# Kernel optimization log

Measured on AMD Instinct MI355X. Metric: run time of the kernel, lower is better.

## Reference

```python
import jax, jax.numpy as jnp
import numpy as np


def setup_inputs() -> dict:
    key = jax.random.key(0)
    kq, kk, kv = jax.random.split(key, 3)
    B, S, D = 16, 2048, 128
    q = jax.random.normal(kq, (B, S, D), dtype=jnp.float32)
    k = jax.random.normal(kk, (B, S, D), dtype=jnp.float32)
    v = jax.random.normal(kv, (B, S, D), dtype=jnp.float32)
    return {"q": q, "k": k, "v": v}


def reference(q, k, v):
    # q: (B, Sq, Dk), k: (B, Skv, Dk), v: (B, Skv, Dv)
    d_k = k.shape[-1]
    scale = 1.0 / jnp.sqrt(jnp.asarray(d_k, dtype=q.dtype))
    scores = jnp.einsum("bqd,bkd->bqk", q, k) * scale  # (B, Sq, Skv)
    # causal mask: strictly-upper-triangular positions set to -inf (mask=True in init)
    Sq = q.shape[-2]
    causal = jnp.triu(jnp.ones((Sq, Sq), dtype=bool), k=1)
    scores = jnp.where(causal, -jnp.inf, scores)
    attn = jax.nn.softmax(scores, axis=-1)
    return jnp.einsum("bqk,bkd->bqd", attn, v)
```

## Files before the change

kernel.cpp:

```cpp
#include <hip/hip_runtime.h>
#include <hip/hip_bf16.h>

typedef __bf16 bf16;
typedef bf16 bf16x8 __attribute__((ext_vector_type(8)));
typedef bf16 bf16x4 __attribute__((ext_vector_type(4)));
typedef float f32x4 __attribute__((ext_vector_type(4)));

#define DHEAD 128
#define SCL2 0.1275500811965365f
#define NINF (-__builtin_inff())

__device__ __forceinline__ unsigned pk2(float a, float b) {
  bf16 x = (bf16)a, y = (bf16)b;
  unsigned short ux = __builtin_bit_cast(unsigned short, x);
  unsigned short uy = __builtin_bit_cast(unsigned short, y);
  return ((unsigned)uy << 16) | (unsigned)ux;
}

__global__ __launch_bounds__(256) void fa_fwd(
    const float* __restrict__ Q, const float* __restrict__ K,
    const float* __restrict__ V, float* __restrict__ O, int S)
{
  const int bid = blockIdx.x;
  const int prb = bid & 255;
  const int hb  = bid >> 8;
  const int b   = prb & 15;
  const int jj  = prb >> 4;
  const int qt  = hb ? jj : (31 - jj);

  const int tid  = threadIdx.x;
  const int wave = tid >> 6;
  const int lane = tid & 63;
  const int lr   = lane & 15;
  const int lg   = lane >> 4;

  __shared__ bf16 Ks[2][32][136];
  __shared__ bf16 Vt[2][DHEAD][40];
  __shared__ bf16 Ps[4][16][40];

  const size_t bo = (size_t)b * S * DHEAD;
  const float* Qb = Q + bo + (size_t)qt * 64 * DHEAD;
  const float* Kb = K + bo;
  const float* Vb = V + bo;
  const int wrow0 = qt * 64 + wave * 16;

  const int j   = tid & 31;
  const int prw = tid >> 5;
  const int d4  = j << 2;
  const int Gw  = (j >> 1) & 3;

  bf16x8 qf[4];
  {
    const float* qr = Qb + (size_t)(wave * 16 + lr) * DHEAD;
    #pragma unroll
    for (int c = 0; c < 4; ++c) {
      const float4 u0 = *reinterpret_cast<const float4*>(qr + c * 32 + lg * 8);
      const float4 u1 = *reinterpret_cast<const float4*>(qr + c * 32 + lg * 8 + 4);
      bf16x8 f;
      f[0] = (bf16)u0.x; f[1] = (bf16)u0.y; f[2] = (bf16)u0.z; f[3] = (bf16)u0.w;
      f[4] = (bf16)u1.x; f[5] = (bf16)u1.y; f[6] = (bf16)u1.z; f[7] = (bf16)u1.w;
      qf[c] = f;
    }
  }

  f32x4 oacc[8];
  #pragma unroll
  for (int i = 0; i < 8; ++i) oacc[i] = (f32x4){0.f, 0.f, 0.f, 0.f};
  float m = NINF, l = 0.f;

  const int nt = 2 * (qt + 1);
  float4 kA[2], kB[2], vA[2], vB[2];

  auto load_tile = [&](int kc) {
    #pragma unroll
    for (int ps = 0; ps < 2; ++ps) {
      const int kv = kc + 2 * (prw + 8 * ps);
      const float* kp = Kb + (size_t)kv * DHEAD + d4;
      const float* vp = Vb + (size_t)kv * DHEAD + d4;
      kA[ps] = *reinterpret_cast<const float4*>(kp);
      kB[ps] = *reinterpret_cast<const float4*>(kp + DHEAD);
      vA[ps] = *reinterpret_cast<const float4*>(vp);
      vB[ps] = *reinterpret_cast<const float4*>(vp + DHEAD);
    }
  };
  auto write_tile = [&](int buf) {
    #pragma unroll
    for (int ps = 0; ps < 2; ++ps) {
      const int kvp = prw + 8 * ps;
      bf16x4 ka, kb;
      ka[0] = (bf16)kA[ps].x; ka[1] = (bf16)kA[ps].y;
      ka[2] = (bf16)kA[ps].z; ka[3] = (bf16)kA[ps].w;
      kb[0] = (bf16)kB[ps].x; kb[1] = (bf16)kB[ps].y;
      kb[2] = (bf16)kB[ps].z; kb[3] = (bf16)kB[ps].w;
      *reinterpret_cast<bf16x4*>(&Ks[buf][2 * kvp][d4])     = ka;
      *reinterpret_cast<bf16x4*>(&Ks[buf][2 * kvp + 1][d4]) = kb;
      const int pS = kvp ^ (Gw << 2);
      const float* fa = &vA[ps].x;
      const float* fb = &vB[ps].x;
      #pragma unroll
      for (int c = 0; c < 4; ++c) {
        *reinterpret_cast<unsigned*>(&Vt[buf][d4 + c][2 * pS]) = pk2(fa[c], fb[c]);
      }
    }
  };

  load_tile(0);
  write_tile(0);
  if (nt > 1) load_tile(32);

  int cur = 0;
  for (int t = 0; t < nt; ++t) {
    __syncthreads();
    if (t + 1 < nt) write_tile(cur ^ 1);
    if (t + 2 < nt) load_tile((t + 2) * 32);

    const int kc = t * 32;
    if (kc <= wrow0 + 15) {
      f32x4 s0 = {0.f, 0.f, 0.f, 0.f}, s1 = {0.f, 0.f, 0.f, 0.f};
      __builtin_amdgcn_s_setprio(1);
      #pragma unroll
      for (int c = 0; c < 4; ++c) {
        const bf16x8 kf0 = *reinterpret_cast<const bf16x8*>(&Ks[cur][lr][c * 32 + lg * 8]);
        const bf16x8 kf1 = *reinterpret_cast<const bf16x8*>(&Ks[cur][16 + lr][c * 32 + lg * 8]);
        s0 = __builtin_amdgcn_mfma_f32_16x16x32_bf16(kf0, qf[c], s0, 0, 0, 0);
        s1 = __builtin_amdgcn_mfma_f32_16x16x32_bf16(kf1, qf[c], s1, 0, 0, 0);
      }
      __builtin_amdgcn_s_setprio(0);

      const int qg = wrow0 + lr;
      float x0[4], x1[4];
      if (kc + 31 > wrow0) {
        #pragma unroll
        for (int r = 0; r < 4; ++r) {
          x0[r] = (kc + 4 * lg + r      > qg) ? NINF : s0[r] * SCL2;
          x1[r] = (kc + 16 + 4 * lg + r > qg) ? NINF : s1[r] * SCL2;
        }
      } else {
        #pragma unroll
        for (int r = 0; r < 4; ++r) { x0[r] = s0[r] * SCL2; x1[r] = s1[r] * SCL2; }
      }
      float tm = NINF;
      #pragma unroll
      for (int r = 0; r < 4; ++r) tm = fmaxf(tm, fmaxf(x0[r], x1[r]));
      tm = fmaxf(tm, __shfl_xor(tm, 16));
      tm = fmaxf(tm, __shfl_xor(tm, 32));

      if (!__all(tm <= m + 8.0f)) {
        const float mn = fmaxf(m, tm);
        const float al = __builtin_exp2f(m - mn);
        m = mn; l *= al;
        #pragma unroll
        for (int r = 0; r < 4; ++r) {
          const float ar = __shfl(al, 4 * lg + r);
          #pragma unroll
          for (int ds = 0; ds < 8; ++ds) oacc[ds][r] *= ar;
        }
      }

      float p0[4], p1[4];
      float ts = 0.f;
      #pragma unroll
      for (int r = 0; r < 4; ++r) {
        p0[r] = __builtin_exp2f(x0[r] - m);
        p1[r] = __builtin_exp2f(x1[r] - m);
        ts += p0[r] + p1[r];
      }
      ts += __shfl_xor(ts, 16);
      ts += __shfl_xor(ts, 32);
      l += ts;

      *reinterpret_cast<unsigned*>(&Ps[wave][lr][4 * lg])          = pk2(p0[0], p0[1]);
      *reinterpret_cast<unsigned*>(&Ps[wave][lr][4 * lg + 2])      = pk2(p0[2], p0[3]);
      *reinterpret_cast<unsigned*>(&Ps[wave][lr][16 + 4 * lg])     = pk2(p1[0], p1[1]);
      *reinterpret_cast<unsigned*>(&Ps[wave][lr][16 + 4 * lg + 2]) = pk2(p1[2], p1[3]);

      const bf16x8 pf = *reinterpret_cast<const bf16x8*>(&Ps[wave][lr][lg * 8]);
      __builtin_amdgcn_s_setprio(1);
      #pragma unroll
      for (int ds = 0; ds < 8; ++ds) {
        const int G = (2 * ds + (lr >> 3)) & 3;
        const bf16x8 vf = *reinterpret_cast<const bf16x8*>(&Vt[cur][ds * 16 + lr][8 * (lg ^ G)]);
        oacc[ds] = __builtin_amdgcn_mfma_f32_16x16x32_bf16(pf, vf, oacc[ds], 0, 0, 0);
      }
      __builtin_amdgcn_s_setprio(0);
    }
    cur ^= 1;
  }

  const float linv = 1.0f / l;
  float* Ob = O + bo + (size_t)(qt * 64 + wave * 16) * DHEAD;
  #pragma unroll
  for (int r = 0; r < 4; ++r) {
    const float ir = __shfl(linv, 4 * lg + r);
    #pragma unroll
    for (int ds = 0; ds < 8; ++ds) {
      Ob[(size_t)(4 * lg + r) * DHEAD + ds * 16 + lr] = oacc[ds][r] * ir;
    }
  }
}

extern "C" void kernel_launch(void* const* d_in, const int* in_sizes, int n_in,
                              void* d_out, int out_size, void* d_ws, size_t ws_size,
                              hipStream_t stream) {
  const float* q = (const float*)d_in[0];
  const float* k = (const float*)d_in[1];
  const float* v = (const float*)d_in[2];
  float* o = (float*)d_out;

  const int B = 16;
  const int S = in_sizes[0] / (B * DHEAD);

  dim3 grid(512);
  dim3 block(256);
  fa_fwd<<<grid, block, 0, stream>>>(q, k, v, o, S);
}
```

Measured before the change: 162.7 us.

## Split KV range across two blocks per query tile and merge partial results

Adds a split-KV path: each query tile's causal KV range is divided between two blocks (1024 blocks total), each writing unnormalized accumulators plus per-row max and sum to workspace. A second kernel merges the two partials with log-sum-exp rescaling and normalizes the output. This is meant to raise occupancy and balance load across CUs on the mi355x. The cost is extra workspace traffic (about 32MB written and read back) and a second launch. It falls back to the original kernel when the workspace is too small or S is not 2048.

```diff
diff --git a/kernel.cpp b/kernel.cpp
--- a/kernel.cpp
+++ b/kernel.cpp
@@ -17,16 +17,25 @@
   return ((unsigned)uy << 16) | (unsigned)ux;
 }
 
-__global__ __launch_bounds__(256) void fa_fwd(
+#define ACC_FLOATS (1024 * 64 * 128)
+#define ML_OFF ACC_FLOATS
+#define WS_NEED ((size_t)(ACC_FLOATS + 1024 * 64 * 2) * 4)
+
+__global__ __launch_bounds__(256) void fa_split(
     const float* __restrict__ Q, const float* __restrict__ K,
-    const float* __restrict__ V, float* __restrict__ O, int S)
+    const float* __restrict__ V, float* __restrict__ ws, int S)
 {
-  const int bid = blockIdx.x;
-  const int prb = bid & 255;
-  const int hb  = bid >> 8;
-  const int b   = prb & 15;
-  const int jj  = prb >> 4;
-  const int qt  = hb ? jj : (31 - jj);
+  const int bid  = blockIdx.x;
+  const int r    = bid >> 8;
+  const int i    = bid & 255;
+  const int b    = i & 15;
+  const int idx  = i >> 4;
+  const int qt   = (r < 2) ? (31 - idx) : idx;
+  const int half = r & 1;
+  const int blk  = bid;
+
+  const int t0 = half * (qt + 1);
+  const int t1 = t0 + (qt + 1);
 
   const int tid  = threadIdx.x;
   const int wave = tid >> 6;
@@ -65,12 +74,10 @@
 
   f32x4 oacc[8];
   #pragma unroll
-  for (int i = 0; i < 8; ++i) oacc[i] = (f32x4){0.f, 0.f, 0.f, 0.f};
+  for (int ii = 0; ii < 8; ++ii) oacc[ii] = (f32x4){0.f, 0.f, 0.f, 0.f};
   float m = NINF, l = 0.f;
 
-  const int nt = 2 * (qt + 1);
   float4 kA[2], kB[2], vA[2], vB[2];
-
   auto load_tile = [&](int kc) {
     #pragma unroll
     for (int ps = 0; ps < 2; ++ps) {
@@ -104,6 +111,232 @@
     }
   };
 
+  load_tile(t0 * 32);
+  write_tile(0);
+  if (t0 + 1 < t1) load_tile((t0 + 1) * 32);
+
+  int cur = 0;
+  for (int t = t0; t < t1; ++t) {
+    __syncthreads();
+    if (t + 1 < t1) write_tile(cur ^ 1);
+    if (t + 2 < t1) load_tile((t + 2) * 32);
+
+    const int kc = t * 32;
+    if (kc <= wrow0 + 15) {
+      f32x4 s0 = {0.f, 0.f, 0.f, 0.f}, s1 = {0.f, 0.f, 0.f, 0.f};
+      __builtin_amdgcn_s_setprio(1);
+      #pragma unroll
+      for (int c = 0; c < 4; ++c) {
+        const bf16x8 kf0 = *reinterpret_cast<const bf16x8*>(&Ks[cur][lr][c * 32 + lg * 8]);
+        const bf16x8 kf1 = *reinterpret_cast<const bf16x8*>(&Ks[cur][16 + lr][c * 32 + lg * 8]);
+        s0 = __builtin_amdgcn_mfma_f32_16x16x32_bf16(kf0, qf[c], s0, 0, 0, 0);
+        s1 = __builtin_amdgcn_mfma_f32_16x16x32_bf16(kf1, qf[c], s1, 0, 0, 0);
+      }
+      __builtin_amdgcn_s_setprio(0);
+
+      const int qg = wrow0 + lr;
+      float x0[4], x1[4];
+      if (kc + 31 > wrow0) {
+        #pragma unroll
+        for (int rr = 0; rr < 4; ++rr) {
+          x0[rr] = (kc + 4 * lg + rr      > qg) ? NINF : s0[rr] * SCL2;
+          x1[rr] = (kc + 16 + 4 * lg + rr > qg) ? NINF : s1[rr] * SCL2;
+        }
+      } else {
+        #pragma unroll
+        for (int rr = 0; rr < 4; ++rr) { x0[rr] = s0[rr] * SCL2; x1[rr] = s1[rr] * SCL2; }
+      }
+      float tm = NINF;
+      #pragma unroll
+      for (int rr = 0; rr < 4; ++rr) tm = fmaxf(tm, fmaxf(x0[rr], x1[rr]));
+      tm = fmaxf(tm, __shfl_xor(tm, 16));
+      tm = fmaxf(tm, __shfl_xor(tm, 32));
+
+      if (!__all(tm <= m + 8.0f)) {
+        const float mn = fmaxf(m, tm);
+        const float al = __builtin_exp2f(m - mn);
+        m = mn; l *= al;
+        #pragma unroll
+        for (int rr = 0; rr < 4; ++rr) {
+          const float ar = __shfl(al, 4 * lg + rr);
+          #pragma unroll
+          for (int ds = 0; ds < 8; ++ds) oacc[ds][rr] *= ar;
+        }
+      }
+
+      float p0[4], p1[4];
+      float ts = 0.f;
+      #pragma unroll
+      for (int rr = 0; rr < 4; ++rr) {
+        p0[rr] = __builtin_exp2f(x0[rr] - m);
+        p1[rr] = __builtin_exp2f(x1[rr] - m);
+        ts += p0[rr] + p1[rr];
+      }
+      ts += __shfl_xor(ts, 16);
+      ts += __shfl_xor(ts, 32);
+      l += ts;
+
+      *reinterpret_cast<unsigned*>(&Ps[wave][lr][4 * lg])          = pk2(p0[0], p0[1]);
+      *reinterpret_cast<unsigned*>(&Ps[wave][lr][4 * lg + 2])      = pk2(p0[2], p0[3]);
+      *reinterpret_cast<unsigned*>(&Ps[wave][lr][16 + 4 * lg])     = pk2(p1[0], p1[1]);
+      *reinterpret_cast<unsigned*>(&Ps[wave][lr][16 + 4 * lg + 2]) = pk2(p1[2], p1[3]);
+
+      const bf16x8 pf = *reinterpret_cast<const bf16x8*>(&Ps[wave][lr][lg * 8]);
+      __builtin_amdgcn_s_setprio(1);
+      #pragma unroll
+      for (int ds = 0; ds < 8; ++ds) {
+        const int G = (2 * ds + (lr >> 3)) & 3;
+        const bf16x8 vf = *reinterpret_cast<const bf16x8*>(&Vt[cur][ds * 16 + lr][8 * (lg ^ G)]);
+        oacc[ds] = __builtin_amdgcn_mfma_f32_16x16x32_bf16(pf, vf, oacc[ds], 0, 0, 0);
+      }
+      __builtin_amdgcn_s_setprio(0);
+    }
+    cur ^= 1;
+  }
+
+  float* aw = ws + (size_t)blk * 8192 + (size_t)(wave * 16) * 128;
+  #pragma unroll
+  for (int rr = 0; rr < 4; ++rr) {
+    #pragma unroll
+    for (int ds = 0; ds < 8; ++ds) {
+      aw[(4 * lg + rr) * 128 + ds * 16 + lr] = oacc[ds][rr];
+    }
+  }
+  if (lg == 0) {
+    float* mlp = ws + ML_OFF + (size_t)(blk * 64 + wave * 16 + lr) * 2;
+    mlp[0] = m;
+    mlp[1] = l;
+  }
+}
+
+__global__ __launch_bounds__(256) void fa_merge(
+    const float* __restrict__ ws, float* __restrict__ O, int S)
+{
+  const int blk2 = blockIdx.x;
+  const int b  = blk2 >> 5;
+  const int qt = blk2 & 31;
+  const int tid = threadIdx.x;
+  const int row = tid >> 2;
+  const int c0  = (tid & 3) * 32;
+
+  const int idx  = (qt >= 16) ? (31 - qt) : qt;
+  const int base = (qt >= 16) ? 0 : 512;
+  const int blk0 = base + (idx << 4) + b;
+  const int blk1 = blk0 + 256;
+
+  const float* ml0 = ws + ML_OFF + (size_t)(blk0 * 64 + row) * 2;
+  const float* ml1 = ws + ML_OFF + (size_t)(blk1 * 64 + row) * 2;
+  const float m0 = ml0[0], l0 = ml0[1];
+  const float m1 = ml1[0], l1 = ml1[1];
+  const float mm = fmaxf(m0, m1);
+  const float a0 = __builtin_exp2f(m0 - mm);
+  const float a1 = __builtin_exp2f(m1 - mm);
+  const float inv = 1.0f / (a0 * l0 + a1 * l1);
+
+  const float* w0 = ws + (size_t)blk0 * 8192 + (size_t)row * 128 + c0;
+  const float* w1 = ws + (size_t)blk1 * 8192 + (size_t)row * 128 + c0;
+  float* out = O + ((size_t)b * S + qt * 64 + row) * DHEAD + c0;
+
+  #pragma unroll
+  for (int qd = 0; qd < 8; ++qd) {
+    const float4 u0 = *reinterpret_cast<const float4*>(w0 + qd * 4);
+    const float4 u1 = *reinterpret_cast<const float4*>(w1 + qd * 4);
+    float4 o;
+    o.x = (a0 * u0.x + a1 * u1.x) * inv;
+    o.y = (a0 * u0.y + a1 * u1.y) * inv;
+    o.z = (a0 * u0.z + a1 * u1.z) * inv;
+    o.w = (a0 * u0.w + a1 * u1.w) * inv;
+    *reinterpret_cast<float4*>(out + qd * 4) = o;
+  }
+}
+
+__global__ __launch_bounds__(256) void fa_fwd(
+    const float* __restrict__ Q, const float* __restrict__ K,
+    const float* __restrict__ V, float* __restrict__ O, int S)
+{
+  const int bid = blockIdx.x;
+  const int prb = bid & 255;
+  const int hb  = bid >> 8;
+  const int b   = prb & 15;
+  const int jj  = prb >> 4;
+  const int qt  = hb ? jj : (31 - jj);
+
+  const int tid  = threadIdx.x;
+  const int wave = tid >> 6;
+  const int lane = tid & 63;
+  const int lr   = lane & 15;
+  const int lg   = lane >> 4;
+
+  __shared__ bf16 Ks[2][32][136];
+  __shared__ bf16 Vt[2][DHEAD][40];
+  __shared__ bf16 Ps[4][16][40];
+
+  const size_t bo = (size_t)b * S * DHEAD;
+  const float* Qb = Q + bo + (size_t)qt * 64 * DHEAD;
+  const float* Kb = K + bo;
+  const float* Vb = V + bo;
+  const int wrow0 = qt * 64 + wave * 16;
+
+  const int j   = tid & 31;
+  const int prw = tid >> 5;
+  const int d4  = j << 2;
+  const int Gw  = (j >> 1) & 3;
+
+  bf16x8 qf[4];
+  {
+    const float* qr = Qb + (size_t)(wave * 16 + lr) * DHEAD;
+    #pragma unroll
+    for (int c = 0; c < 4; ++c) {
+      const float4 u0 = *reinterpret_cast<const float4*>(qr + c * 32 + lg * 8);
+      const float4 u1 = *reinterpret_cast<const float4*>(qr + c * 32 + lg * 8 + 4);
+      bf16x8 f;
+      f[0] = (bf16)u0.x; f[1] = (bf16)u0.y; f[2] = (bf16)u0.z; f[3] = (bf16)u0.w;
+      f[4] = (bf16)u1.x; f[5] = (bf16)u1.y; f[6] = (bf16)u1.z; f[7] = (bf16)u1.w;
+      qf[c] = f;
+    }
+  }
+
+  f32x4 oacc[8];
+  #pragma unroll
+  for (int ii = 0; ii < 8; ++ii) oacc[ii] = (f32x4){0.f, 0.f, 0.f, 0.f};
+  float m = NINF, l = 0.f;
+
+  const int nt = 2 * (qt + 1);
+  float4 kA[2], kB[2], vA[2], vB[2];
+
+  auto load_tile = [&](int kc) {
+    #pragma unroll
+    for (int ps = 0; ps < 2; ++ps) {
+      const int kv = kc + 2 * (prw + 8 * ps);
+      const float* kp = Kb + (size_t)kv * DHEAD + d4;
+      const float* vp = Vb + (size_t)kv * DHEAD + d4;
+      kA[ps] = *reinterpret_cast<const float4*>(kp);
+      kB[ps] = *reinterpret_cast<const float4*>(kp + DHEAD);
+      vA[ps] = *reinterpret_cast<const float4*>(vp);
+      vB[ps] = *reinterpret_cast<const float4*>(vp + DHEAD);
+    }
+  };
+  auto write_tile = [&](int buf) {
+    #pragma unroll
+    for (int ps = 0; ps < 2; ++ps) {
+      const int kvp = prw + 8 * ps;
+      bf16x4 ka, kb;
+      ka[0] = (bf16)kA[ps].x; ka[1] = (bf16)kA[ps].y;
+      ka[2] = (bf16)kA[ps].z; ka[3] = (bf16)kA[ps].w;
+      kb[0] = (bf16)kB[ps].x; kb[1] = (bf16)kB[ps].y;
+      kb[2] = (bf16)kB[ps].z; kb[3] = (bf16)kB[ps].w;
+      *reinterpret_cast<bf16x4*>(&Ks[buf][2 * kvp][d4])     = ka;
+      *reinterpret_cast<bf16x4*>(&Ks[buf][2 * kvp + 1][d4]) = kb;
+      const int pS = kvp ^ (Gw << 2);
+      const float* fa = &vA[ps].x;
+      const float* fb = &vB[ps].x;
+      #pragma unroll
+      for (int c = 0; c < 4; ++c) {
+        *reinterpret_cast<unsigned*>(&Vt[buf][d4 + c][2 * pS]) = pk2(fa[c], fb[c]);
+      }
+    }
+  };
+
   load_tile(0);
   write_tile(0);
   if (nt > 1) load_tile(32);
@@ -131,17 +364,17 @@
       float x0[4], x1[4];
       if (kc + 31 > wrow0) {
         #pragma unroll
-        for (int r = 0; r < 4; ++r) {
-          x0[r] = (kc + 4 * lg + r      > qg) ? NINF : s0[r] * SCL2;
-          x1[r] = (kc + 16 + 4 * lg + r > qg) ? NINF : s1[r] * SCL2;
+        for (int rr = 0; rr < 4; ++rr) {
+          x0[rr] = (kc + 4 * lg + rr      > qg) ? NINF : s0[rr] * SCL2;
+          x1[rr] = (kc + 16 + 4 * lg + rr > qg) ? NINF : s1[rr] * SCL2;
         }
       } else {
         #pragma unroll
-        for (int r = 0; r < 4; ++r) { x0[r] = s0[r] * SCL2; x1[r] = s1[r] * SCL2; }
+        for (int rr = 0; rr < 4; ++rr) { x0[rr] = s0[rr] * SCL2; x1[rr] = s1[rr] * SCL2; }
       }
       float tm = NINF;
       #pragma unroll
-      for (int r = 0; r < 4; ++r) tm = fmaxf(tm, fmaxf(x0[r], x1[r]));
+      for (int rr = 0; rr < 4; ++rr) tm = fmaxf(tm, fmaxf(x0[rr], x1[rr]));
       tm = fmaxf(tm, __shfl_xor(tm, 16));
       tm = fmaxf(tm, __shfl_xor(tm, 32));
 
@@ -150,20 +383,20 @@
         const float al = __builtin_exp2f(m - mn);
         m = mn; l *= al;
         #pragma unroll
-        for (int r = 0; r < 4; ++r) {
-          const float ar = __shfl(al, 4 * lg + r);
+        for (int rr = 0; rr < 4; ++rr) {
+          const float ar = __shfl(al, 4 * lg + rr);
           #pragma unroll
-          for (int ds = 0; ds < 8; ++ds) oacc[ds][r] *= ar;
+          for (int ds = 0; ds < 8; ++ds) oacc[ds][rr] *= ar;
         }
       }
 
       float p0[4], p1[4];
       float ts = 0.f;
       #pragma unroll
-      for (int r = 0; r < 4; ++r) {
-        p0[r] = __builtin_exp2f(x0[r] - m);
-        p1[r] = __builtin_exp2f(x1[r] - m);
-        ts += p0[r] + p1[r];
+      for (int rr = 0; rr < 4; ++rr) {
+        p0[rr] = __builtin_exp2f(x0[rr] - m);
+        p1[rr] = __builtin_exp2f(x1[rr] - m);
+        ts += p0[rr] + p1[rr];
       }
       ts += __shfl_xor(ts, 16);
       ts += __shfl_xor(ts, 32);
@@ -190,11 +423,11 @@
   const float linv = 1.0f / l;
   float* Ob = O + bo + (size_t)(qt * 64 + wave * 16) * DHEAD;
   #pragma unroll
-  for (int r = 0; r < 4; ++r) {
-    const float ir = __shfl(linv, 4 * lg + r);
+  for (int rr = 0; rr < 4; ++rr) {
+    const float ir = __shfl(linv, 4 * lg + rr);
     #pragma unroll
     for (int ds = 0; ds < 8; ++ds) {
-      Ob[(size_t)(4 * lg + r) * DHEAD + ds * 16 + lr] = oacc[ds][r] * ir;
+      Ob[(size_t)(4 * lg + rr) * DHEAD + ds * 16 + lr] = oacc[ds][rr] * ir;
     }
   }
 }
@@ -210,7 +443,11 @@
   const int B = 16;
   const int S = in_sizes[0] / (B * DHEAD);
 
-  dim3 grid(512);
-  dim3 block(256);
-  fa_fwd<<<grid, block, 0, stream>>>(q, k, v, o, S);
+  if (ws_size >= WS_NEED && S == 2048) {
+    float* ws = (float*)d_ws;
+    fa_split<<<dim3(1024), dim3(256), 0, stream>>>(q, k, v, ws, S);
+    fa_merge<<<dim3(512), dim3(256), 0, stream>>>(ws, o, S);
+  } else {
+    fa_fwd<<<dim3(512), dim3(256), 0, stream>>>(q, k, v, o, S);
+  }
 }
```

Measured after the change: 161.1 us. Within noise of the previous version (-1.0%).
